# Performance work log

Hardware: AMD Instinct MI355X
Metric: run time of the kernel (lower is better)

## Reference

```python
import jax, jax.numpy as jnp
import numpy as np

EPS = 1e-6
B, CIN, COUT, N, S, M1, M2 = 4, 32, 32, 8192, 8, 12, 12
X, Y = 2 * M1 + 1, 2 * M2 + 1


def setup_inputs() -> dict:
    key = jax.random.key(0)
    ks = jax.random.split(key, 20)
    x = jax.random.normal(ks[0], (B, CIN, N), dtype=jnp.float32)
    loc = jax.random.uniform(ks[1], (B, N, 2), dtype=jnp.float32)
    # per-batch permutation of point indices; equal-size subdomains of N//S points
    ind = jnp.stack([jax.random.permutation(k, N) for k in jax.random.split(ks[2], B)]).astype(jnp.int32)
    ss = 1.0 / S
    sc = 1.0 / (CIN * COUT)
    u = lambda k, shp, s: s * jax.random.uniform(k, shp, dtype=jnp.float32)
    inp = {
        'x': x, 'loc': loc, 'ind': ind,
        'w1s_re': u(ks[3], (S, X, M2), ss), 'w1s_im': u(ks[4], (S, X, M2), ss),
        'w2s_re': u(ks[5], (S, M1 + 1, 1), ss), 'w2s_im': u(ks[6], (S, M1 + 1, 1), ss),
        'w1_re': u(ks[7], (CIN, COUT, X, M2), sc), 'w1_im': u(ks[8], (CIN, COUT, X, M2), sc),
        'w2_re': u(ks[9], (CIN, COUT, M1 + 1, 1), sc), 'w2_im': u(ks[10], (CIN, COUT, M1 + 1, 1), sc),
        'w1sb_re': u(ks[11], (S, X, M2), ss), 'w1sb_im': u(ks[12], (S, X, M2), ss),
        'w2sb_re': u(ks[13], (S, M1 + 1, 1), ss), 'w2sb_im': u(ks[14], (S, M1 + 1, 1), ss),
    }
    return inp


def _forward(x, loc, ind, w1s, w2s, w1, w2, w1sb, w2sb):
    b, cin, n = x.shape
    s, xg_dim, m2 = w1s.shape
    m1 = (xg_dim - 1) // 2
    xx, yy = 2 * m1 + 1, 2 * m2 + 1
    p = n // s
    norm = jnp.asarray(1.0 / np.sqrt(xx * yy), jnp.float32)

    # gather per-subdomain points (equal partitions replace the sep ragged split)
    xg = jnp.take_along_axis(x, ind[:, None, :], axis=2).reshape(b, cin, s, p)
    locg = jnp.take_along_axis(loc, ind[:, :, None], axis=1).reshape(b, s, p, 2)

    # per-subdomain min-max normalization of coords to [-pi, pi]
    om = jnp.swapaxes(locg, -1, -2)                      # [b,s,2,p]
    om = om - om.min(-1, keepdims=True)
    om = om / (om.max(-1, keepdims=True) + EPS)
    om = om * (2.0 * jnp.pi) - jnp.pi

    kx = (jnp.arange(xx) - m1).astype(jnp.float32)
    ky = (jnp.arange(yy) - m2).astype(jnp.float32)
    # exact (type-1) NUDFT basis; conj-wrapped adjoint = sum_p d_p exp(-i k.omega_p)
    E1 = jnp.exp(-1j * om[:, :, 0, :, None] * kx)        # [b,s,p,X]
    E2 = jnp.exp(-1j * om[:, :, 1, :, None] * ky)        # [b,s,p,Y]

    coef = jnp.einsum('bcsp,bspx,bspy->bcsxy', xg.astype(jnp.complex64), E1, E2) * norm

    i1 = coef[..., :m2]                                  # [b,c,s,X,m2]
    i2 = coef[:, :, :, :m1 + 1, m2:m2 + 1]               # [b,c,s,m1+1,1]

    i1 = jnp.einsum('bisxy,sxy->bixy', i1, w1s)
    i2 = jnp.einsum('bisxy,sxy->bixy', i2, w2s)
    i1 = jnp.einsum('bixy,ioxy->boxy', i1, w1)
    i2 = jnp.einsum('bixy,ioxy->boxy', i2, w2)
    i1 = jnp.einsum('boxy,sxy->bosxy', i1, w1sb)
    i2 = jnp.einsum('boxy,sxy->bosxy', i2, w2sb)

    cout = i1.shape[1]
    full = jnp.zeros((b, cout, s, xx, yy), jnp.complex64)
    full = full.at[..., :m2].set(i1)
    full = full.at[..., yy - m2:].set(jnp.conj(i1[..., ::-1, ::-1]))
    full = full.at[..., xx - m1 - 1:, m2:m2 + 1].set(jnp.conj(i2[..., ::-1, ::-1]))
    full = full.at[..., :m1 + 1, m2:m2 + 1].set(i2)      # overwrites center row (mode 0)

    # conj-wrapped forward NUFFT: sum_k c_k exp(+i k.omega_p)
    outc = jnp.einsum('bcsxy,bspx,bspy->bcsp', full, jnp.conj(E1), jnp.conj(E2)) * norm
    outr = outc.real                                     # [b,cout,s,p]

    # per-subdomain min-max renormalization back to input data range
    t = outr - outr.min(-1, keepdims=True)
    t = t / (t.max(-1, keepdims=True) + EPS)
    mn = xg.min(-1, keepdims=True)
    mx = xg.max(-1, keepdims=True)
    vals = t * (mx - mn) + mn                            # needs cin == cout

    # scatter back: output[b,:,ind[b,j]] = vals[b,:,j]
    inv = jnp.argsort(ind, axis=1)
    return jnp.take_along_axis(vals.reshape(b, cout, n), inv[:, None, :], axis=2)


def reference(x, loc, ind, w1s_re, w1s_im, w2s_re, w2s_im, w1_re, w1_im,
              w2_re, w2_im, w1sb_re, w1sb_im, w2sb_re, w2sb_im):
    c = lambda re, im: (re + 1j * im).astype(jnp.complex64)
    return _forward(x, loc, ind, c(w1s_re, w1s_im), c(w2s_re, w2s_im),
                    c(w1_re, w1_im), c(w2_re, w2_im),
                    c(w1sb_re, w1sb_im), c(w2sb_re, w2sb_im))
```

## Files before the change

### kernel.cpp

```cpp
#include <hip/hip_runtime.h>

#define B_ 4
#define C_ 32
#define N_ 8192
#define S_ 8
#define P_ 1024
#define NM_FWD 325
#define NM_INV 313
#define NORM_F 0.04f

#define PI_F 3.14159265358979f
#define TWOPI_F 6.28318530717959f

__device__ __forceinline__ float blk_red(float v, float* red, bool is_min){
  int tid = threadIdx.x;
  red[tid] = v; __syncthreads();
  for (int off = blockDim.x >> 1; off > 0; off >>= 1){
    if (tid < off) red[tid] = is_min ? fminf(red[tid], red[tid+off]) : fmaxf(red[tid], red[tid+off]);
    __syncthreads();
  }
  float r = red[0]; __syncthreads();
  return r;
}

__global__ __launch_bounds__(256) void k_om(const float* __restrict__ loc,
                                            const int* __restrict__ ind,
                                            float* __restrict__ om){
  int b = blockIdx.x >> 3, s = blockIdx.x & 7;
  int tid = threadIdx.x;
  __shared__ float l0[P_], l1[P_];
  __shared__ float red[256];
  const int* indb = ind + b*N_ + s*P_;
  float mn0=1e30f, mx0=-1e30f, mn1=1e30f, mx1=-1e30f;
  for (int p = tid; p < P_; p += 256){
    int n = indb[p];
    float a = loc[(b*N_ + n)*2];
    float c = loc[(b*N_ + n)*2 + 1];
    l0[p] = a; l1[p] = c;
    mn0 = fminf(mn0, a); mx0 = fmaxf(mx0, a);
    mn1 = fminf(mn1, c); mx1 = fmaxf(mx1, c);
  }
  mn0 = blk_red(mn0, red, true);  mx0 = blk_red(mx0, red, false);
  mn1 = blk_red(mn1, red, true);  mx1 = blk_red(mx1, red, false);
  float i0 = TWOPI_F / (mx0 - mn0 + 1e-6f);
  float i1 = TWOPI_F / (mx1 - mn1 + 1e-6f);
  float* om0 = om + ((b*S_ + s)*2)*P_;
  float* om1 = om0 + P_;
  for (int p = tid; p < P_; p += 256){
    om0[p] = (l0[p] - mn0)*i0 - PI_F;
    om1[p] = (l1[p] - mn1)*i1 - PI_F;
  }
}

__global__ __launch_bounds__(512) void k_xg(const float* __restrict__ x,
                                            const int* __restrict__ ind,
                                            float* __restrict__ xg_t,
                                            float* __restrict__ pmm){
  int blk = blockIdx.x;
  int part = blk & 3, bs = blk >> 2;
  int b = bs >> 3, s = bs & 7;
  int t = threadIdx.x;
  int c = t & 31, pl = t >> 5;
  __shared__ int inds[256];
  __shared__ float rmn[8*32], rmx[8*32];
  if (t < 256) inds[t] = ind[b*N_ + s*P_ + part*256 + t];
  __syncthreads();
  const float* xr = x + (b*C_ + c)*N_;
  float mn = 1e30f, mx = -1e30f;
  int pbase = part*256;
  for (int k = 0; k < 16; ++k){
    int pp = pl + k*16;
    float v = xr[inds[pp]];
    xg_t[(bs*P_ + pbase + pp)*C_ + c] = v;
    mn = fminf(mn, v); mx = fmaxf(mx, v);
  }
  mn = fminf(mn, __shfl_xor(mn, 32));
  mx = fmaxf(mx, __shfl_xor(mx, 32));
  int wid = t >> 6;
  if ((t & 63) < 32){ rmn[wid*32 + c] = mn; rmx[wid*32 + c] = mx; }
  __syncthreads();
  if (t < 32){
    float m0 = rmn[t], M0 = rmx[t];
    #pragma unroll
    for (int w = 1; w < 8; ++w){ m0 = fminf(m0, rmn[w*32+t]); M0 = fmaxf(M0, rmx[w*32+t]); }
    pmm[((bs*4 + part)*32 + t)*2]     = m0;
    pmm[((bs*4 + part)*32 + t)*2 + 1] = M0;
  }
}

__global__ __launch_bounds__(448) void k_fwd(const float* __restrict__ om,
                                             const float* __restrict__ xg_t,
                                             float* __restrict__ coef_part){
  int blk = blockIdx.x;
  int part = blk & 1;
  int tile = (blk >> 1) % 6;
  int bs   = blk / 12;
  int t = threadIdx.x;
  int ml = t >> 3;
  int q  = t & 7;
  int mf = tile*56 + ml;
  int mfc = min(mf, NM_FWD-1);
  int xo = mfc / 13, yo = mfc - xo*13;
  float kx = (float)(xo - 12), ky = (float)(yo - 12);
  __shared__ float o0s[512], o1s[512];
  __shared__ __align__(16) float xgs[64*32];
  __shared__ float Wre[56*68], Wim[56*68];
  const float* om0 = om + bs*2*P_;
  const float* om1 = om0 + P_;
  for (int i = t; i < 512; i += 448){
    o0s[i] = om0[part*512 + i];
    o1s[i] = om1[part*512 + i];
  }
  float ar[4] = {0,0,0,0}, ai[4] = {0,0,0,0};
  for (int ch = 0; ch < 8; ++ch){
    int pbase = part*512 + ch*64;
    __syncthreads();
    for (int i = t; i < 512; i += 448){
      ((float4*)xgs)[i] = ((const float4*)xg_t)[(bs*P_ + pbase + (i>>3))*8 + (i&7)];
    }
    {
      int ps = t & 7;
      #pragma unroll
      for (int k = 0; k < 8; ++k){
        int p = ps + k*8;
        float th = o0s[ch*64 + p]*kx + o1s[ch*64 + p]*ky;
        float sn, cs; __sincosf(th, &sn, &cs);
        Wre[ml*68 + p] = cs;
        Wim[ml*68 + p] = sn;
      }
    }
    __syncthreads();
    #pragma unroll 8
    for (int p = 0; p < 64; ++p){
      float4 g4 = *(const float4*)&xgs[p*32 + q*4];
      float wre = Wre[ml*68 + p], wim = Wim[ml*68 + p];
      ar[0] += g4.x*wre; ai[0] += g4.x*wim;
      ar[1] += g4.y*wre; ai[1] += g4.y*wim;
      ar[2] += g4.z*wre; ai[2] += g4.z*wim;
      ar[3] += g4.w*wre; ai[3] += g4.w*wim;
    }
  }
  if (mf < NM_FWD){
    float* dst = coef_part + (size_t)((part*32 + bs)*NM_FWD + mf)*64 + q*8;
    #pragma unroll
    for (int j = 0; j < 4; ++j){
      dst[j*2]     = ar[j]*NORM_F;
      dst[j*2 + 1] = -ai[j]*NORM_F;
    }
  }
}

__global__ __launch_bounds__(64) void k_mid(const float* __restrict__ coef_part,
    const float* __restrict__ w1s_re, const float* __restrict__ w1s_im,
    const float* __restrict__ w2s_re, const float* __restrict__ w2s_im,
    const float* __restrict__ w1_re,  const float* __restrict__ w1_im,
    const float* __restrict__ w2_re,  const float* __restrict__ w2_im,
    const float* __restrict__ w1sb_re,const float* __restrict__ w1sb_im,
    const float* __restrict__ w2sb_re,const float* __restrict__ w2sb_im,
    float* __restrict__ zbuf){
  int blk = blockIdx.x;
  int b = blk / NM_INV, q = blk - b*NM_INV;
  int lane = threadIdx.x;
  int o = lane & 31;
  int hi = lane >> 5;
  bool p1 = (q < 300);
  int x = p1 ? q/12 : q - 300;
  int y = p1 ? q - (q/12)*12 : 12;
  int mf = x*13 + y;
  __shared__ float iv[64];
  float are = 0.f, aim = 0.f;
  for (int s = 0; s < 8; ++s){
    const float* cp = coef_part + (size_t)((hi*32 + b*8 + s)*NM_FWD + mf)*64 + o*2;
    float cre = cp[0], cim = cp[1];
    float wre, wim;
    if (p1){ int wi = (s*25+x)*12+y; wre = w1s_re[wi]; wim = w1s_im[wi]; }
    else   { int wi = s*13+x;        wre = w2s_re[wi]; wim = w2s_im[wi]; }
    are += cre*wre - cim*wim;
    aim += cre*wim + cim*wre;
  }
  are += __shfl_xor(are, 32);
  aim += __shfl_xor(aim, 32);
  if (hi == 0){ iv[o*2] = are; iv[o*2+1] = aim; }
  __syncthreads();
  float ore = 0.f, oim = 0.f;
  for (int ii = 0; ii < 16; ++ii){
    int i = hi*16 + ii;
    float zre = iv[i*2], zim = iv[i*2+1];
    float wre, wim;
    if (p1){ int wi = ((i*32 + o)*25 + x)*12 + y; wre = w1_re[wi]; wim = w1_im[wi]; }
    else   { int wi = (i*32 + o)*13 + x;          wre = w2_re[wi]; wim = w2_im[wi]; }
    ore += zre*wre - zim*wim;
    oim += zre*wim + zim*wre;
  }
  ore += __shfl_xor(ore, 32);
  oim += __shfl_xor(oim, 32);
  for (int si = 0; si < 4; ++si){
    int s = hi*4 + si;
    float wre, wim, scale;
    if (p1){ int wi = (s*25+x)*12+y; wre = w1sb_re[wi]; wim = w1sb_im[wi]; scale = 0.08f; }
    else   { int wi = s*13+x;        wre = w2sb_re[wi]; wim = w2sb_im[wi]; scale = (x==12)?0.04f:0.08f; }
    float zre = (ore*wre - oim*wim)*scale;
    float zim = (ore*wim + oim*wre)*scale;
    size_t oi = (size_t)((b*8 + s)*NM_INV + q)*64 + o*2;
    zbuf[oi] = zre; zbuf[oi+1] = zim;
  }
}

__global__ __launch_bounds__(512) void k_inv(const float* __restrict__ om,
                                             const float* __restrict__ zbuf,
                                             float* __restrict__ routc){
  int blk = blockIdx.x;
  int pt = blk & 15, bs = blk >> 4;
  int p0 = pt*64;
  int t = threadIdx.x;
  int oq = t >> 6, pl = t & 63;
  __shared__ float o0s[64], o1s[64];
  __shared__ float F1[64*66], F2[64*66];
  __shared__ __align__(16) float Zs[64*64];
  const float* om0 = om + bs*2*P_;
  if (t < 64) o0s[t] = om0[p0 + t];
  else if (t < 128) o1s[t-64] = om0[P_ + p0 + t - 64];
  float acc[4] = {0,0,0,0};
  for (int chv = 0; chv < 5; ++chv){
    int m0 = chv*64;
    __syncthreads();
    for (int i = t; i < 4096; i += 512){
      int m = i >> 6, rest = i & 63;
      Zs[i] = (m0 + m < NM_INV) ? zbuf[(size_t)(bs*NM_INV + m0 + m)*64 + rest] : 0.f;
    }
    {
      int ml = t >> 3, ps = t & 7;
      int mg = min(m0 + ml, NM_INV-1);
      float kx, ky;
      if (mg < 300){ int xx = mg/12; kx = (float)(xx - 12); ky = (float)(mg - xx*12 - 12); }
      else { kx = (float)(mg - 312); ky = 0.f; }
      #pragma unroll
      for (int k = 0; k < 8; ++k){
        int p = ps + k*8;
        float th = o0s[p]*kx + o1s[p]*ky;
        float sn, cs; __sincosf(th, &sn, &cs);
        F1[ml*66 + p] = cs;
        F2[ml*66 + p] = sn;
      }
    }
    __syncthreads();
    #pragma unroll 4
    for (int m = 0; m < 64; ++m){
      float f1 = F1[m*66 + pl], f2 = F2[m*66 + pl];
      float4 za = *(const float4*)&Zs[m*64 + oq*8];
      float4 zb = *(const float4*)&Zs[m*64 + oq*8 + 4];
      acc[0] += za.x*f1 - za.y*f2;
      acc[1] += za.z*f1 - za.w*f2;
      acc[2] += zb.x*f1 - zb.y*f2;
      acc[3] += zb.z*f1 - zb.w*f2;
    }
  }
  #pragma unroll
  for (int j = 0; j < 4; ++j){
    routc[(size_t)(bs*C_ + oq*4 + j)*P_ + p0 + pl] = acc[j];
  }
}

__global__ __launch_bounds__(256) void k_fin(const float* __restrict__ routc,
                                             const float* __restrict__ pmm,
                                             const int* __restrict__ ind,
                                             float* __restrict__ out){
  int blk = blockIdx.x;
  int o = blk & 31, s = (blk >> 5) & 7, b = blk >> 8;
  int bs = b*8 + s;
  int t = threadIdx.x;
  __shared__ float red[256];
  const float* rr = routc + (size_t)(bs*C_ + o)*P_;
  float v[4]; float mn = 1e30f, mx = -1e30f;
  #pragma unroll
  for (int k = 0; k < 4; ++k){
    v[k] = rr[t + k*256];
    mn = fminf(mn, v[k]); mx = fmaxf(mx, v[k]);
  }
  mn = blk_red(mn, red, true);
  mx = blk_red(mx, red, false);
  float xmn = 1e30f, xmx = -1e30f;
  #pragma unroll
  for (int part = 0; part < 4; ++part){
    xmn = fminf(xmn, pmm[((bs*4+part)*32 + o)*2]);
    xmx = fmaxf(xmx, pmm[((bs*4+part)*32 + o)*2 + 1]);
  }
  float scale = (xmx - xmn) / (mx - mn + 1e-6f);
  const int* indb = ind + b*N_ + s*P_;
  float* outb = out + (size_t)(b*C_ + o)*N_;
  #pragma unroll
  for (int k = 0; k < 4; ++k){
    int p = t + k*256;
    outb[indb[p]] = (v[k] - mn)*scale + xmn;
  }
}

extern "C" void kernel_launch(void* const* d_in, const int* in_sizes, int n_in,
                              void* d_out, int out_size, void* d_ws, size_t ws_size,
                              hipStream_t stream){
  const float* x      = (const float*)d_in[0];
  const float* loc    = (const float*)d_in[1];
  const int*   ind    = (const int*)  d_in[2];
  const float* w1s_re = (const float*)d_in[3];
  const float* w1s_im = (const float*)d_in[4];
  const float* w2s_re = (const float*)d_in[5];
  const float* w2s_im = (const float*)d_in[6];
  const float* w1_re  = (const float*)d_in[7];
  const float* w1_im  = (const float*)d_in[8];
  const float* w2_re  = (const float*)d_in[9];
  const float* w2_im  = (const float*)d_in[10];
  const float* w1sb_re= (const float*)d_in[11];
  const float* w1sb_im= (const float*)d_in[12];
  const float* w2sb_re= (const float*)d_in[13];
  const float* w2sb_im= (const float*)d_in[14];
  float* out = (float*)d_out;

  float* ws = (float*)d_ws;
  float* om        = ws;
  float* xg_t      = om + 65536;
  float* pmm       = xg_t + 1048576;
  float* coef_part = pmm + 8192;
  float* zbuf      = coef_part + 1331200;
  float* routc     = xg_t;

  k_om <<<32,   256, 0, stream>>>(loc, ind, om);
  k_xg <<<128,  512, 0, stream>>>(x, ind, xg_t, pmm);
  k_fwd<<<384,  448, 0, stream>>>(om, xg_t, coef_part);
  k_mid<<<4*NM_INV, 64, 0, stream>>>(coef_part, w1s_re, w1s_im, w2s_re, w2s_im,
                                     w1_re, w1_im, w2_re, w2_im,
                                     w1sb_re, w1sb_im, w2sb_re, w2sb_im, zbuf);
  k_inv<<<512,  512, 0, stream>>>(om, zbuf, routc);
  k_fin<<<1024, 256, 0, stream>>>(routc, pmm, ind, out);
}
```

Baseline: 210.7 us.

## Use twiddle recurrence in inverse NUDFT, pre-transpose spectral weights, reorder modes

```diff
diff --git a/kernel.cpp b/kernel.cpp
--- a/kernel.cpp
+++ b/kernel.cpp
@@ -68,6 +68,7 @@
   const float* xr = x + (b*C_ + c)*N_;
   float mn = 1e30f, mx = -1e30f;
   int pbase = part*256;
+  #pragma unroll 4
   for (int k = 0; k < 16; ++k){
     int pp = pl + k*16;
     float v = xr[inds[pp]];
@@ -85,6 +86,36 @@
     for (int w = 1; w < 8; ++w){ m0 = fminf(m0, rmn[w*32+t]); M0 = fmaxf(M0, rmx[w*32+t]); }
     pmm[((bs*4 + part)*32 + t)*2]     = m0;
     pmm[((bs*4 + part)*32 + t)*2 + 1] = M0;
+  }
+}
+
+__global__ __launch_bounds__(256) void k_wt(
+    const float* __restrict__ w1s_re, const float* __restrict__ w1s_im,
+    const float* __restrict__ w2s_re, const float* __restrict__ w2s_im,
+    const float* __restrict__ w1_re,  const float* __restrict__ w1_im,
+    const float* __restrict__ w2_re,  const float* __restrict__ w2_im,
+    const float* __restrict__ w1sb_re,const float* __restrict__ w1sb_im,
+    const float* __restrict__ w2sb_re,const float* __restrict__ w2sb_im,
+    float* __restrict__ w1t, float* __restrict__ w1st, float* __restrict__ w1sbt){
+  int q = blockIdx.x;
+  int t = threadIdx.x;
+  bool p1 = (q < 300);
+  int x = p1 ? q % 25 : q - 300;
+  int y = p1 ? q / 25 : 12;
+  for (int idx = t; idx < 1024; idx += 256){
+    float wre, wim;
+    if (p1){ int wi = (idx*25 + x)*12 + y; wre = w1_re[wi]; wim = w1_im[wi]; }
+    else   { int wi = idx*13 + x;          wre = w2_re[wi]; wim = w2_im[wi]; }
+    w1t[(size_t)(q*1024 + idx)*2]     = wre;
+    w1t[(size_t)(q*1024 + idx)*2 + 1] = wim;
+  }
+  if (t < 8){
+    int s = t;
+    float a, b2, c2, d2;
+    if (p1){ int wi = (s*25+x)*12+y; a=w1s_re[wi]; b2=w1s_im[wi]; c2=w1sb_re[wi]; d2=w1sb_im[wi]; }
+    else   { int wi = s*13+x;        a=w2s_re[wi]; b2=w2s_im[wi]; c2=w2sb_re[wi]; d2=w2sb_im[wi]; }
+    w1st[(q*8+s)*2]   = a;  w1st[(q*8+s)*2+1]  = b2;
+    w1sbt[(q*8+s)*2]  = c2; w1sbt[(q*8+s)*2+1] = d2;
   }
 }
 
@@ -151,30 +182,24 @@
 }
 
 __global__ __launch_bounds__(64) void k_mid(const float* __restrict__ coef_part,
-    const float* __restrict__ w1s_re, const float* __restrict__ w1s_im,
-    const float* __restrict__ w2s_re, const float* __restrict__ w2s_im,
-    const float* __restrict__ w1_re,  const float* __restrict__ w1_im,
-    const float* __restrict__ w2_re,  const float* __restrict__ w2_im,
-    const float* __restrict__ w1sb_re,const float* __restrict__ w1sb_im,
-    const float* __restrict__ w2sb_re,const float* __restrict__ w2sb_im,
-    float* __restrict__ zbuf){
+    const float* __restrict__ w1t, const float* __restrict__ w1st,
+    const float* __restrict__ w1sbt, float* __restrict__ zbuf){
   int blk = blockIdx.x;
   int b = blk / NM_INV, q = blk - b*NM_INV;
   int lane = threadIdx.x;
   int o = lane & 31;
   int hi = lane >> 5;
   bool p1 = (q < 300);
-  int x = p1 ? q/12 : q - 300;
-  int y = p1 ? q - (q/12)*12 : 12;
+  int x = p1 ? q % 25 : q - 300;
+  int y = p1 ? q / 25 : 12;
   int mf = x*13 + y;
   __shared__ float iv[64];
   float are = 0.f, aim = 0.f;
+  #pragma unroll
   for (int s = 0; s < 8; ++s){
     const float* cp = coef_part + (size_t)((hi*32 + b*8 + s)*NM_FWD + mf)*64 + o*2;
     float cre = cp[0], cim = cp[1];
-    float wre, wim;
-    if (p1){ int wi = (s*25+x)*12+y; wre = w1s_re[wi]; wim = w1s_im[wi]; }
-    else   { int wi = s*13+x;        wre = w2s_re[wi]; wim = w2s_im[wi]; }
+    float wre = w1st[(q*8+s)*2], wim = w1st[(q*8+s)*2+1];
     are += cre*wre - cim*wim;
     aim += cre*wim + cim*wre;
   }
@@ -183,22 +208,22 @@
   if (hi == 0){ iv[o*2] = are; iv[o*2+1] = aim; }
   __syncthreads();
   float ore = 0.f, oim = 0.f;
+  #pragma unroll
   for (int ii = 0; ii < 16; ++ii){
     int i = hi*16 + ii;
     float zre = iv[i*2], zim = iv[i*2+1];
-    float wre, wim;
-    if (p1){ int wi = ((i*32 + o)*25 + x)*12 + y; wre = w1_re[wi]; wim = w1_im[wi]; }
-    else   { int wi = (i*32 + o)*13 + x;          wre = w2_re[wi]; wim = w2_im[wi]; }
+    const float* wp = w1t + (size_t)(q*1024 + i*32 + o)*2;
+    float wre = wp[0], wim = wp[1];
     ore += zre*wre - zim*wim;
     oim += zre*wim + zim*wre;
   }
   ore += __shfl_xor(ore, 32);
   oim += __shfl_xor(oim, 32);
+  float scale = p1 ? 0.08f : ((x==12) ? 0.04f : 0.08f);
+  #pragma unroll
   for (int si = 0; si < 4; ++si){
     int s = hi*4 + si;
-    float wre, wim, scale;
-    if (p1){ int wi = (s*25+x)*12+y; wre = w1sb_re[wi]; wim = w1sb_im[wi]; scale = 0.08f; }
-    else   { int wi = s*13+x;        wre = w2sb_re[wi]; wim = w2sb_im[wi]; scale = (x==12)?0.04f:0.08f; }
+    float wre = w1sbt[(q*8+s)*2], wim = w1sbt[(q*8+s)*2+1];
     float zre = (ore*wre - oim*wim)*scale;
     float zim = (ore*wim + oim*wre)*scale;
     size_t oi = (size_t)((b*8 + s)*NM_INV + q)*64 + o*2;
@@ -206,7 +231,7 @@
   }
 }
 
-__global__ __launch_bounds__(512) void k_inv(const float* __restrict__ om,
+__global__ __launch_bounds__(256) void k_inv(const float* __restrict__ om,
                                              const float* __restrict__ zbuf,
                                              float* __restrict__ routc){
   int blk = blockIdx.x;
@@ -214,51 +239,55 @@
   int p0 = pt*64;
   int t = threadIdx.x;
   int oq = t >> 6, pl = t & 63;
-  __shared__ float o0s[64], o1s[64];
-  __shared__ float F1[64*66], F2[64*66];
   __shared__ __align__(16) float Zs[64*64];
-  const float* om0 = om + bs*2*P_;
-  if (t < 64) o0s[t] = om0[p0 + t];
-  else if (t < 128) o1s[t-64] = om0[P_ + p0 + t - 64];
-  float acc[4] = {0,0,0,0};
+  const float* zb = zbuf + (size_t)bs*NM_INV*64;
+  float o0 = om[bs*2*P_ + p0 + pl];
+  float o1 = om[bs*2*P_ + P_ + p0 + pl];
+  float d0s, d0c; __sincosf(o0, &d0s, &d0c);
+  float d1s, d1c; __sincosf(o1, &d1s, &d1c);
+  float rs0, rc0; __sincosf(12.f*(o0+o1), &rs0, &rc0);
+  float rre = rc0, rim = -rs0;
+  float fre = rre, fim = rim;
+  int rowc = 0;
+  float acc[8] = {0,0,0,0,0,0,0,0};
   for (int chv = 0; chv < 5; ++chv){
     int m0 = chv*64;
-    __syncthreads();
-    for (int i = t; i < 4096; i += 512){
-      int m = i >> 6, rest = i & 63;
-      Zs[i] = (m0 + m < NM_INV) ? zbuf[(size_t)(bs*NM_INV + m0 + m)*64 + rest] : 0.f;
-    }
-    {
-      int ml = t >> 3, ps = t & 7;
-      int mg = min(m0 + ml, NM_INV-1);
-      float kx, ky;
-      if (mg < 300){ int xx = mg/12; kx = (float)(xx - 12); ky = (float)(mg - xx*12 - 12); }
-      else { kx = (float)(mg - 312); ky = 0.f; }
-      #pragma unroll
-      for (int k = 0; k < 8; ++k){
-        int p = ps + k*8;
-        float th = o0s[p]*kx + o1s[p]*ky;
-        float sn, cs; __sincosf(th, &sn, &cs);
-        F1[ml*66 + p] = cs;
-        F2[ml*66 + p] = sn;
+    int mcount = min(64, NM_INV - m0);
+    __syncthreads();
+    for (int i = t*4; i < mcount*64; i += 1024)
+      *(float4*)&Zs[i] = *(const float4*)&zb[m0*64 + i];
+    __syncthreads();
+    const float* zrow = Zs + oq*16;
+    for (int m = 0; m < mcount; ++m){
+      if (rowc == 25){
+        float nr = rre*d1c - rim*d1s;
+        float ni = rre*d1s + rim*d1c;
+        rre = nr; rim = ni;
+        fre = rre; fim = rim;
+        rowc = 0;
       }
-    }
-    __syncthreads();
-    #pragma unroll 4
-    for (int m = 0; m < 64; ++m){
-      float f1 = F1[m*66 + pl], f2 = F2[m*66 + pl];
-      float4 za = *(const float4*)&Zs[m*64 + oq*8];
-      float4 zb = *(const float4*)&Zs[m*64 + oq*8 + 4];
-      acc[0] += za.x*f1 - za.y*f2;
-      acc[1] += za.z*f1 - za.w*f2;
-      acc[2] += zb.x*f1 - zb.y*f2;
-      acc[3] += zb.z*f1 - zb.w*f2;
-    }
-  }
-  #pragma unroll
-  for (int j = 0; j < 4; ++j){
-    routc[(size_t)(bs*C_ + oq*4 + j)*P_ + p0 + pl] = acc[j];
-  }
+      float4 za = *(const float4*)&zrow[m*64];
+      float4 zb4 = *(const float4*)&zrow[m*64 + 4];
+      float4 zc = *(const float4*)&zrow[m*64 + 8];
+      float4 zd = *(const float4*)&zrow[m*64 + 12];
+      acc[0] += za.x*fre  - za.y*fim;
+      acc[1] += za.z*fre  - za.w*fim;
+      acc[2] += zb4.x*fre - zb4.y*fim;
+      acc[3] += zb4.z*fre - zb4.w*fim;
+      acc[4] += zc.x*fre  - zc.y*fim;
+      acc[5] += zc.z*fre  - zc.w*fim;
+      acc[6] += zd.x*fre  - zd.y*fim;
+      acc[7] += zd.z*fre  - zd.w*fim;
+      float nf = fre*d0c - fim*d0s;
+      float ni = fre*d0s + fim*d0c;
+      fre = nf; fim = ni;
+      ++rowc;
+    }
+  }
+  float* outp = routc + (size_t)(bs*C_ + oq*8)*P_ + p0 + pl;
+  #pragma unroll
+  for (int j = 0; j < 8; ++j)
+    outp[(size_t)j*P_] = acc[j];
 }
 
 __global__ __launch_bounds__(256) void k_fin(const float* __restrict__ routc,
@@ -321,14 +350,19 @@
   float* pmm       = xg_t + 1048576;
   float* coef_part = pmm + 8192;
   float* zbuf      = coef_part + 1331200;
+  float* w1t       = zbuf + 641024;
+  float* w1st      = w1t + 641024;
+  float* w1sbt     = w1st + 5008;
   float* routc     = xg_t;
 
   k_om <<<32,   256, 0, stream>>>(loc, ind, om);
   k_xg <<<128,  512, 0, stream>>>(x, ind, xg_t, pmm);
+  k_wt <<<NM_INV, 256, 0, stream>>>(w1s_re, w1s_im, w2s_re, w2s_im,
+                                    w1_re, w1_im, w2_re, w2_im,
+                                    w1sb_re, w1sb_im, w2sb_re, w2sb_im,
+                                    w1t, w1st, w1sbt);
   k_fwd<<<384,  448, 0, stream>>>(om, xg_t, coef_part);
-  k_mid<<<4*NM_INV, 64, 0, stream>>>(coef_part, w1s_re, w1s_im, w2s_re, w2s_im,
-                                     w1_re, w1_im, w2_re, w2_im,
-                                     w1sb_re, w1sb_im, w2sb_re, w2sb_im, zbuf);
-  k_inv<<<512,  512, 0, stream>>>(om, zbuf, routc);
+  k_mid<<<4*NM_INV, 64, 0, stream>>>(coef_part, w1t, w1st, w1sbt, zbuf);
+  k_inv<<<512,  256, 0, stream>>>(om, zbuf, routc);
   k_fin<<<1024, 256, 0, stream>>>(routc, pmm, ind, out);
 }
```

Result: no change. 209.6 us (-0.5%).
